# Optimization experiments

Hardware: AMD Instinct MI355X
Metric: run time of the kernel (lower is better)

Reference implementation:

```python
import jax, jax.numpy as jnp
import numpy as np

B = 16
Dv, Hv, Wv = 128, 128, 128   # patchsize voxel grid (C=1)
NPTS = 1920                  # 16*120 points
EPS_IN = 1e-5                # InstanceNorm eps


def _inorm(x):
    # InstanceNorm1d, affine=False: normalize over last (length) dim per (b, c)
    m = jnp.mean(x, axis=-1, keepdims=True)
    v = jnp.var(x, axis=-1, keepdims=True)
    return (x - m) * jax.lax.rsqrt(v + EPS_IN)


def _mlp(q, w1, b1, w2, b2, w3, b3, w4, b4, w5, b5):
    b = q.shape[0]
    x = q.reshape(b, 256, 8)                                    # (b, 2048//8, 8)
    x = jnp.einsum('bil,oi->bol', x, w1) + b1[None, :, None]    # Conv1d(256,240,1) -> (b,240,8)
    x = jax.nn.relu(_inorm(x.reshape(b, 64, 30)))               # view (b,64,30), IN(64)
    # Conv1d(64,128,1,groups=64): each in-ch -> 2 out-chs; then view (b,32,120)
    x = (x[:, :, None, :] * w2[None, :, :, None] + b2.reshape(1, 64, 2, 1)).reshape(b, 32, 120)
    x = jax.nn.relu(_inorm(x))
    # Conv1d(32,64,1,groups=32); view (b,16,480)
    x = (x[:, :, None, :] * w3[None, :, :, None] + b3.reshape(1, 32, 2, 1)).reshape(b, 16, 480)
    x = jax.nn.relu(_inorm(x))
    # Conv1d(16,64,1,groups=16); view (b,16,1920)
    x = (x[:, :, None, :] * w4[None, :, :, None] + b4.reshape(1, 16, 4, 1)).reshape(b, 16, 1920)
    x = jax.nn.relu(_inorm(x))
    return jnp.einsum('bil,oi->bol', x, w5) + b5[None, :, None]  # Conv1d(16,3,1) -> (b,3,1920)


def _splat(vals, grid):
    # True adjoint of 3D grid_sample (align_corners=False, zeros padding):
    # trilinear scatter-add of point values into the voxel grid.
    # vals: (b, N); grid: (b, N, 3) with (x, y, z) ~ (W, H, D) normalized coords.
    b, n = vals.shape
    px = ((grid[..., 0] + 1.0) * Wv - 1.0) * 0.5
    py = ((grid[..., 1] + 1.0) * Hv - 1.0) * 0.5
    pz = ((grid[..., 2] + 1.0) * Dv - 1.0) * 0.5
    x0f = jnp.floor(px); y0f = jnp.floor(py); z0f = jnp.floor(pz)
    fx = px - x0f; fy = py - y0f; fz = pz - z0f
    x0 = x0f.astype(jnp.int32); y0 = y0f.astype(jnp.int32); z0 = z0f.astype(jnp.int32)
    bidx = jnp.arange(b, dtype=jnp.int32)[:, None]
    out = jnp.zeros(b * Dv * Hv * Wv, dtype=vals.dtype)
    for dz in (0, 1):
        wz = fz if dz else (1.0 - fz)
        for dy in (0, 1):
            wy = fy if dy else (1.0 - fy)
            for dx in (0, 1):
                wx = fx if dx else (1.0 - fx)
                xi = x0 + dx; yi = y0 + dy; zi = z0 + dz
                w = wx * wy * wz * vals
                valid = (xi >= 0) & (xi < Wv) & (yi >= 0) & (yi < Hv) & (zi >= 0) & (zi < Dv)
                w = jnp.where(valid, w, 0.0)
                xi = jnp.clip(xi, 0, Wv - 1)
                yi = jnp.clip(yi, 0, Hv - 1)
                zi = jnp.clip(zi, 0, Dv - 1)
                flat = ((bidx * Dv + zi) * Hv + yi) * Wv + xi
                out = out.at[flat.ravel()].add(w.ravel())
    return out.reshape(b, 1, Dv, Hv, Wv)


def _avgpool3(x):
    # AvgPool3d(3, stride=1, padding=1, count_include_pad=True) as separable 1D averages
    for ax in (2, 3, 4):
        pad = [(1, 1) if i == ax else (0, 0) for i in range(5)]
        xp = jnp.pad(x, pad)
        n = x.shape[ax]
        x = (jax.lax.slice_in_dim(xp, 0, n, axis=ax)
             + jax.lax.slice_in_dim(xp, 1, n + 1, axis=ax)
             + jax.lax.slice_in_dim(xp, 2, n + 2, axis=ax)) / 3.0
    return x


def _smooth(x):
    return _avgpool3(_avgpool3(_avgpool3(x)))


def _forward(q, q_val, w1, b1, w2, b2, w3, b3, w4, b4, w5, b5):
    b = q.shape[0]
    q3 = _mlp(q, w1, b1, w2, b2, w3, b3, w4, b4, w5, b5)   # (b, 3, 1920)
    coords = jnp.tanh(q3)                                    # q0_coord
    grid = jnp.transpose(coords, (0, 2, 1))                  # (b, 1920, 3)
    vals = jnp.broadcast_to(jax.nn.sigmoid(q_val).reshape(1, NPTS), (b, NPTS))
    out = _splat(vals, grid)
    out0 = _splat(jnp.ones((b, NPTS), q.dtype), grid)
    return _smooth(out) / (_smooth(out0) + 0.001)


def setup_inputs() -> dict:
    key = jax.random.key(0)
    ks = jax.random.split(key, 12)
    sc = 0.1
    return {
        'q': jax.random.normal(ks[0], (B, 2048), jnp.float32),
        'q_val': jax.random.normal(ks[1], (1, 1, 16, 120), jnp.float32),
        'w1': jax.random.normal(ks[2], (240, 256), jnp.float32) * sc,
        'b1': jax.random.normal(ks[3], (240,), jnp.float32) * sc,
        'w2': jax.random.normal(ks[4], (64, 2), jnp.float32) * sc,
        'b2': jax.random.normal(ks[5], (128,), jnp.float32) * sc,
        'w3': jax.random.normal(ks[6], (32, 2), jnp.float32) * sc,
        'b3': jax.random.normal(ks[7], (64,), jnp.float32) * sc,
        'w4': jax.random.normal(ks[8], (16, 4), jnp.float32) * sc,
        'b4': jax.random.normal(ks[9], (64,), jnp.float32) * sc,
        'w5': jax.random.normal(ks[10], (3, 16), jnp.float32) * sc,
        'b5': jax.random.normal(ks[11], (3,), jnp.float32) * sc,
    }


def reference(q, q_val, w1, b1, w2, b2, w3, b3, w4, b4, w5, b5):
    return _forward(q, q_val, w1, b1, w2, b2, w3, b3, w4, b4, w5, b5)
```

## Files before the change

### kernel.cpp

```cpp
#include <hip/hip_runtime.h>
#include <cstddef>

#define NB 16
#define NVOX 128
#define NPT 1920
#define NPAIRS 32768

static __device__ __forceinline__ float2 f2(float a, float b) {
    float2 r; r.x = a; r.y = b; return r;
}

__global__ __launch_bounds__(256)
void zero_out(float4* __restrict__ out)
{
    int idx = blockIdx.x * 2048 + threadIdx.x;
    #pragma unroll
    for (int i = 0; i < 8; ++i)
        out[idx + i * 256] = make_float4(0.f, 0.f, 0.f, 0.f);
}

__global__ __launch_bounds__(256)
void mlp_stage1(const float* __restrict__ q, const float* __restrict__ w1,
                const float* __restrict__ b1, float* __restrict__ x1g)
{
    __shared__ float wrow[256];
    __shared__ float psum[256];
    const int o = blockIdx.x;
    const int t = threadIdx.x;

    wrow[t] = w1[o * 256 + t];
    __syncthreads();

    const int half = t >> 7;
    const int bl = t & 127;
    const int b = bl >> 3, l = bl & 7;
    const float* qb = q + b * 2048 + l + half * 1024;
    float s = 0.f;
    #pragma unroll 8
    for (int i = 0; i < 128; ++i)
        s = fmaf(wrow[half * 128 + i], qb[i * 8], s);
    psum[t] = s;
    __syncthreads();

    if (t < 128) {
        int bb = t >> 3, ll = t & 7;
        x1g[bb * 1920 + o * 8 + ll] = b1[o] + psum[t] + psum[t + 128];
    }
}

__global__ __launch_bounds__(256)
void mlp_tail(const float* __restrict__ x1g, const float* __restrict__ qval,
              const float* __restrict__ w2, const float* __restrict__ b2,
              const float* __restrict__ w3, const float* __restrict__ b3,
              const float* __restrict__ w4, const float* __restrict__ b4,
              const float* __restrict__ w5, const float* __restrict__ b5,
              float4* __restrict__ pts, unsigned char* __restrict__ flags)
{
    __shared__ float bufA[7680];
    __shared__ float bufC[3840];
    __shared__ float psum[256], psq[256];
    __shared__ float meanv[64], rstdv[64];
    __shared__ float m4[16], r4[16];

    const int b = blockIdx.x;
    const int t = threadIdx.x;

    for (int u = t; u < 1920; u += 256) bufA[u] = x1g[b * 1920 + u];
    __syncthreads();

    {
        int c = t >> 2, g = t & 3;
        float s = 0.f, s2 = 0.f;
        for (int p = g; p < 30; p += 4) { float v = bufA[c * 30 + p]; s += v; s2 += v * v; }
        psum[t] = s; psq[t] = s2;
    }
    __syncthreads();
    if (t < 64) {
        float s = 0.f, s2 = 0.f;
        for (int g = 0; g < 4; ++g) { s += psum[t * 4 + g]; s2 += psq[t * 4 + g]; }
        float m = s * (1.f / 30.f);
        float var = s2 * (1.f / 30.f) - m * m;
        meanv[t] = m; rstdv[t] = rsqrtf(var + 1e-5f);
    }
    __syncthreads();
    for (int k = t; k < 1920; k += 256) {
        int c = k / 30;
        bufA[k] = fmaxf((bufA[k] - meanv[c]) * rstdv[c], 0.f);
    }
    __syncthreads();

    for (int m = t; m < 3840; m += 256) {
        int c = m / 60;
        int r = m - c * 60;
        int j = r / 30;
        int p = r - j * 30;
        bufC[m] = fmaf(bufA[c * 30 + p], w2[c * 2 + j], b2[c * 2 + j]);
    }
    __syncthreads();
    {
        int c = t >> 3, g = t & 7;
        float s = 0.f, s2 = 0.f;
        for (int p = g; p < 120; p += 8) { float v = bufC[c * 120 + p]; s += v; s2 += v * v; }
        psum[t] = s; psq[t] = s2;
    }
    __syncthreads();
    if (t < 32) {
        float s = 0.f, s2 = 0.f;
        for (int g = 0; g < 8; ++g) { s += psum[t * 8 + g]; s2 += psq[t * 8 + g]; }
        float m = s * (1.f / 120.f);
        float var = s2 * (1.f / 120.f) - m * m;
        meanv[t] = m; rstdv[t] = rsqrtf(var + 1e-5f);
    }
    __syncthreads();
    for (int m = t; m < 3840; m += 256) {
        int c = m / 120;
        bufC[m] = fmaxf((bufC[m] - meanv[c]) * rstdv[c], 0.f);
    }
    __syncthreads();

    for (int m = t; m < 7680; m += 256) {
        int c = m / 240;
        int r = m - c * 240;
        int j = r / 120;
        int p = r - j * 120;
        bufA[m] = fmaf(bufC[c * 120 + p], w3[c * 2 + j], b3[c * 2 + j]);
    }
    __syncthreads();

    const int c3 = t >> 4, g3 = t & 15;
    {
        float s = 0.f, s2 = 0.f;
        for (int k = 0; k < 30; ++k) { float v = bufA[c3 * 480 + g3 + 16 * k]; s += v; s2 += v * v; }
        psum[t] = s; psq[t] = s2;
    }
    __syncthreads();
    if (t < 16) {
        float s = 0.f, s2 = 0.f;
        for (int g = 0; g < 16; ++g) { s += psum[t * 16 + g]; s2 += psq[t * 16 + g]; }
        float m = s * (1.f / 480.f);
        float var = s2 * (1.f / 480.f) - m * m;
        meanv[t] = m; rstdv[t] = rsqrtf(var + 1e-5f);
    }
    __syncthreads();
    {
        float m = meanv[c3], r = rstdv[c3];
        float s = 0.f, s2 = 0.f;
        for (int k = 0; k < 30; ++k) {
            int idx = c3 * 480 + g3 + 16 * k;
            float v = fmaxf((bufA[idx] - m) * r, 0.f);
            bufA[idx] = v; s += v; s2 += v * v;
        }
        psum[t] = s; psq[t] = s2;
    }
    __syncthreads();
    if (t < 16) {
        float s = 0.f, s2 = 0.f;
        for (int g = 0; g < 16; ++g) { s += psum[t * 16 + g]; s2 += psq[t * 16 + g]; }
        float sum4 = 0.f, sq4 = 0.f;
        for (int j = 0; j < 4; ++j) {
            float w = w4[t * 4 + j], bb = b4[t * 4 + j];
            sum4 += w * s + 480.f * bb;
            sq4  += w * w * s2 + 2.f * w * bb * s + 480.f * bb * bb;
        }
        float m = sum4 * (1.f / 1920.f);
        float var = sq4 * (1.f / 1920.f) - m * m;
        m4[t] = m; r4[t] = rsqrtf(var + 1e-5f);
    }
    __syncthreads();

    for (int l = t; l < NPT; l += 256) {
        int j = l / 480;
        int p = l - j * 480;
        float a0 = b5[0], a1 = b5[1], a2 = b5[2];
        #pragma unroll
        for (int c = 0; c < 16; ++c) {
            float xv = bufA[c * 480 + p];
            float x4 = fmaf(xv, w4[c * 4 + j], b4[c * 4 + j]);
            float h  = fmaxf((x4 - m4[c]) * r4[c], 0.f);
            a0 = fmaf(w5[c],      h, a0);
            a1 = fmaf(w5[16 + c], h, a1);
            a2 = fmaf(w5[32 + c], h, a2);
        }
        float px = tanhf(a0) * 64.f + 63.5f;
        float py = tanhf(a1) * 64.f + 63.5f;
        float pz = tanhf(a2) * 64.f + 63.5f;
        float val = 1.f / (1.f + expf(-qval[l]));

        float4 pv; pv.x = px; pv.y = py; pv.z = pz; pv.w = val;
        pts[b * NPT + l] = pv;

        int x0 = (int)floorf(px), y0 = (int)floorf(py), z0 = (int)floorf(pz);
        int xlo = max(0, x0 - 3), xhi = min(127, x0 + 4);
        int ylo = max(0, y0 - 3), yhi = min(127, y0 + 4);
        int zlo = max(0, z0 - 3), zhi = min(127, z0 + 4);
        if (xlo > xhi || ylo > yhi || zlo > zhi) continue;
        int txl = xlo >> 3, txh = xhi >> 3;
        int tyl = ylo >> 3, tyh = yhi >> 3;
        int tzl = zlo >> 3, tzh = zhi >> 3;
        for (int tz = tzl; tz <= tzh; ++tz)
            for (int ty = tyl; ty <= tyh; ++ty)
                for (int tx = txl; tx <= txh; ++tx)
                    flags[((b * 16 + tz) * 16 + ty) * 16 + tx] = 1;
    }
}

__global__ __launch_bounds__(256)
void compact_tiles(const unsigned char* __restrict__ flags,
                   int* __restrict__ count, int* __restrict__ list)
{
    int i = blockIdx.x * 256 + threadIdx.x;
    const unsigned short* fp = (const unsigned short*)flags;
    if (fp[i] != 0) {
        int pos = atomicAdd(count, 1);
        list[pos] = i;
    }
}

__device__ __forceinline__ void coef(int g, float& cm1, float& c0, float& cp1)
{
    cm1 = (g == 1 || g == 127) ? 5.f : 6.f;
    c0  = (g == 0 || g == 127) ? 4.f : 7.f;
    cp1 = (g == 0 || g == 126) ? 5.f : 6.f;
}

__global__ __launch_bounds__(512)
void tile_active(const float4* __restrict__ pts, const int* __restrict__ count,
                 const int* __restrict__ list, float* __restrict__ out)
{
    __shared__ float2 raw[14 * 14 * 22];
    __shared__ float2 zs[8 * 14 * 22];

    if ((int)blockIdx.x >= *count) return;
    const int code = list[blockIdx.x];
    const int pair = code & 7;
    const int ty   = (code >> 3) & 15;
    const int tz   = (code >> 7) & 15;
    const int b    = code >> 11;
    const int Tx = pair * 16, Ty = ty * 8, Tz = tz * 8;
    const int t = threadIdx.x;

    float* ob = out + (((size_t)(b * NVOX + Tz) * NVOX + Ty) * NVOX + Tx);

    for (int u = t; u < 14 * 14 * 22; u += 512) raw[u] = f2(0.f, 0.f);
    __syncthreads();

    const float4* pb = pts + b * NPT;
    for (int p = t; p < NPT; p += 512) {
        float4 pt = pb[p];
        float x0f = floorf(pt.x), y0f = floorf(pt.y), z0f = floorf(pt.z);
        int x0 = (int)x0f, y0 = (int)y0f, z0 = (int)z0f;
        int lx0 = x0 - Tx + 3, ly0 = y0 - Ty + 3, lz0 = z0 - Tz + 3;
        if (lx0 + 1 < 0 || lx0 > 21 || ly0 + 1 < 0 || ly0 > 13 ||
            lz0 + 1 < 0 || lz0 > 13) continue;
        float fx = pt.x - x0f, fy = pt.y - y0f, fz = pt.z - z0f;
        float val = pt.w;
        #pragma unroll
        for (int dz = 0; dz < 2; ++dz) {
            int zi = z0 + dz, lz = lz0 + dz;
            if ((unsigned)zi >= 128u || (unsigned)lz >= 14u) continue;
            float wz = dz ? fz : 1.f - fz;
            #pragma unroll
            for (int dy = 0; dy < 2; ++dy) {
                int yi = y0 + dy, ly = ly0 + dy;
                if ((unsigned)yi >= 128u || (unsigned)ly >= 14u) continue;
                float wy = dy ? fy : 1.f - fy;
                #pragma unroll
                for (int dx = 0; dx < 2; ++dx) {
                    int xi = x0 + dx, lx = lx0 + dx;
                    if ((unsigned)xi >= 128u || (unsigned)lx >= 22u) continue;
                    float w = (dx ? fx : 1.f - fx) * wy * wz;
                    float2* cell = &raw[(lz * 14 + ly) * 22 + lx];
                    atomicAdd(&cell->x, w * val);
                    atomicAdd(&cell->y, w);
                }
            }
        }
    }
    __syncthreads();

    for (int u = t; u < 8 * 14 * 22; u += 512) {
        int lx = u % 22;
        int tmp = u / 22;
        int ly = tmp % 14;
        int lz = tmp / 14;
        float cm1, c0, cp1; coef(Tz + lz, cm1, c0, cp1);
        const float2* a = &raw[(lz * 14 + ly) * 22 + lx];
        const int S = 14 * 22;
        float sx = (a[0].x + a[6 * S].x) + 3.f * (a[S].x + a[5 * S].x)
                 + cm1 * a[2 * S].x + c0 * a[3 * S].x + cp1 * a[4 * S].x;
        float sy = (a[0].y + a[6 * S].y) + 3.f * (a[S].y + a[5 * S].y)
                 + cm1 * a[2 * S].y + c0 * a[3 * S].y + cp1 * a[4 * S].y;
        zs[u] = f2(sx * (1.f / 27.f), sy * (1.f / 27.f));
    }
    __syncthreads();

    float2* ys = raw;
    for (int u = t; u < 8 * 8 * 22; u += 512) {
        int lx = u % 22;
        int tmp = u / 22;
        int ly = tmp % 8;
        int lz = tmp / 8;
        float cm1, c0, cp1; coef(Ty + ly, cm1, c0, cp1);
        const float2* a = &zs[(lz * 14 + ly) * 22 + lx];
        const int S = 22;
        float sx = (a[0].x + a[6 * S].x) + 3.f * (a[S].x + a[5 * S].x)
                 + cm1 * a[2 * S].x + c0 * a[3 * S].x + cp1 * a[4 * S].x;
        float sy = (a[0].y + a[6 * S].y) + 3.f * (a[S].y + a[5 * S].y)
                 + cm1 * a[2 * S].y + c0 * a[3 * S].y + cp1 * a[4 * S].y;
        ys[(lz * 8 + ly) * 22 + lx] = f2(sx * (1.f / 27.f), sy * (1.f / 27.f));
    }
    __syncthreads();

    for (int u = t; u < 16 * 8 * 8; u += 512) {
        int x = u & 15, y = (u >> 4) & 7, z = u >> 7;
        float cm1, c0, cp1; coef(Tx + x, cm1, c0, cp1);
        const float2* a = &ys[(z * 8 + y) * 22 + x];
        float sx = (a[0].x + a[6].x) + 3.f * (a[1].x + a[5].x)
                 + cm1 * a[2].x + c0 * a[3].x + cp1 * a[4].x;
        float sy = (a[0].y + a[6].y) + 3.f * (a[1].y + a[5].y)
                 + cm1 * a[2].y + c0 * a[3].y + cp1 * a[4].y;
        ob[((size_t)z * NVOX + y) * NVOX + x] =
            (sx * (1.f / 27.f)) / (sy * (1.f / 27.f) + 0.001f);
    }
}

extern "C" void kernel_launch(void* const* d_in, const int* in_sizes, int n_in,
                              void* d_out, int out_size, void* d_ws, size_t ws_size,
                              hipStream_t stream)
{
    const float* q    = (const float*)d_in[0];
    const float* qval = (const float*)d_in[1];
    const float* w1   = (const float*)d_in[2];
    const float* b1   = (const float*)d_in[3];
    const float* w2   = (const float*)d_in[4];
    const float* b2   = (const float*)d_in[5];
    const float* w3   = (const float*)d_in[6];
    const float* b3   = (const float*)d_in[7];
    const float* w4   = (const float*)d_in[8];
    const float* b4   = (const float*)d_in[9];
    const float* w5   = (const float*)d_in[10];
    const float* b5   = (const float*)d_in[11];
    float* out = (float*)d_out;

    unsigned char* flags = (unsigned char*)d_ws;
    int*    count = (int*)((char*)d_ws + 65536);
    int*    list  = (int*)((char*)d_ws + 65552);
    float4* pts   = (float4*)((char*)d_ws + 196624);
    float*  x1g   = (float*)((char*)d_ws + 688144);

    hipMemsetAsync(d_ws, 0, 65540, stream);

    zero_out<<<4096, 256, 0, stream>>>((float4*)out);

    mlp_stage1<<<240, 256, 0, stream>>>(q, w1, b1, x1g);

    mlp_tail<<<NB, 256, 0, stream>>>(x1g, qval, w2, b2, w3, b3,
                                     w4, b4, w5, b5, pts, flags);

    compact_tiles<<<NPAIRS / 256, 256, 0, stream>>>(flags, count, list);

    tile_active<<<NPAIRS, 512, 0, stream>>>(pts, count, list, out);
}
```

Before: 249.4 us.

## Fuse output zeroing and tile compaction into tile kernel; register-sliding smoothing passes

Removes the separate full-output zero kernel and the tile-compaction kernel. Each of the 32768 tile blocks now checks its own flag: inactive tiles write zeros directly and exit, while active tiles run the splat and smoothing. The three separable smoothing passes now run in place in one shared buffer, with each thread sliding a 7-tap register window and the final pass writing float4 stores. This avoids writing the output twice and cuts shared memory use, which may raise occupancy. The cost is a launch of all blocks, including the inactive ones, and some passes that use only a fraction of the threads.

```diff
diff --git a/kernel.cpp b/kernel.cpp
--- a/kernel.cpp
+++ b/kernel.cpp
@@ -8,15 +8,6 @@
 
 static __device__ __forceinline__ float2 f2(float a, float b) {
     float2 r; r.x = a; r.y = b; return r;
-}
-
-__global__ __launch_bounds__(256)
-void zero_out(float4* __restrict__ out)
-{
-    int idx = blockIdx.x * 2048 + threadIdx.x;
-    #pragma unroll
-    for (int i = 0; i < 8; ++i)
-        out[idx + i * 256] = make_float4(0.f, 0.f, 0.f, 0.f);
 }
 
 __global__ __launch_bounds__(256)
@@ -204,18 +195,6 @@
     }
 }
 
-__global__ __launch_bounds__(256)
-void compact_tiles(const unsigned char* __restrict__ flags,
-                   int* __restrict__ count, int* __restrict__ list)
-{
-    int i = blockIdx.x * 256 + threadIdx.x;
-    const unsigned short* fp = (const unsigned short*)flags;
-    if (fp[i] != 0) {
-        int pos = atomicAdd(count, 1);
-        list[pos] = i;
-    }
-}
-
 __device__ __forceinline__ void coef(int g, float& cm1, float& c0, float& cp1)
 {
     cm1 = (g == 1 || g == 127) ? 5.f : 6.f;
@@ -223,15 +202,14 @@
     cp1 = (g == 0 || g == 126) ? 5.f : 6.f;
 }
 
-__global__ __launch_bounds__(512)
-void tile_active(const float4* __restrict__ pts, const int* __restrict__ count,
-                 const int* __restrict__ list, float* __restrict__ out)
+__global__ __launch_bounds__(512, 8)
+void tile_all(const float4* __restrict__ pts,
+              const unsigned char* __restrict__ flags,
+              float* __restrict__ out)
 {
     __shared__ float2 raw[14 * 14 * 22];
-    __shared__ float2 zs[8 * 14 * 22];
-
-    if ((int)blockIdx.x >= *count) return;
-    const int code = list[blockIdx.x];
+
+    const int code = blockIdx.x;
     const int pair = code & 7;
     const int ty   = (code >> 3) & 15;
     const int tz   = (code >> 7) & 15;
@@ -241,7 +219,20 @@
 
     float* ob = out + (((size_t)(b * NVOX + Tz) * NVOX + Ty) * NVOX + Tx);
 
-    for (int u = t; u < 14 * 14 * 22; u += 512) raw[u] = f2(0.f, 0.f);
+    const unsigned short fl = ((const unsigned short*)flags)[code];
+    if (fl == 0) {
+        if (t < 256) {
+            int x4 = t & 3, y = (t >> 2) & 7, z = t >> 5;
+            *(float4*)&ob[((size_t)z * NVOX + y) * NVOX + x4 * 4] =
+                make_float4(0.f, 0.f, 0.f, 0.f);
+        }
+        return;
+    }
+
+    {
+        float4* rz = (float4*)raw;
+        for (int u = t; u < 2156; u += 512) rz[u] = make_float4(0.f, 0.f, 0.f, 0.f);
+    }
     __syncthreads();
 
     const float4* pb = pts + b * NPT;
@@ -278,49 +269,66 @@
     }
     __syncthreads();
 
-    for (int u = t; u < 8 * 14 * 22; u += 512) {
-        int lx = u % 22;
-        int tmp = u / 22;
-        int ly = tmp % 14;
-        int lz = tmp / 14;
-        float cm1, c0, cp1; coef(Tz + lz, cm1, c0, cp1);
-        const float2* a = &raw[(lz * 14 + ly) * 22 + lx];
-        const int S = 14 * 22;
-        float sx = (a[0].x + a[6 * S].x) + 3.f * (a[S].x + a[5 * S].x)
-                 + cm1 * a[2 * S].x + c0 * a[3 * S].x + cp1 * a[4 * S].x;
-        float sy = (a[0].y + a[6 * S].y) + 3.f * (a[S].y + a[5 * S].y)
-                 + cm1 * a[2 * S].y + c0 * a[3 * S].y + cp1 * a[4 * S].y;
-        zs[u] = f2(sx * (1.f / 27.f), sy * (1.f / 27.f));
-    }
-    __syncthreads();
-
-    float2* ys = raw;
-    for (int u = t; u < 8 * 8 * 22; u += 512) {
-        int lx = u % 22;
-        int tmp = u / 22;
-        int ly = tmp % 8;
-        int lz = tmp / 8;
-        float cm1, c0, cp1; coef(Ty + ly, cm1, c0, cp1);
-        const float2* a = &zs[(lz * 14 + ly) * 22 + lx];
-        const int S = 22;
-        float sx = (a[0].x + a[6 * S].x) + 3.f * (a[S].x + a[5 * S].x)
-                 + cm1 * a[2 * S].x + c0 * a[3 * S].x + cp1 * a[4 * S].x;
-        float sy = (a[0].y + a[6 * S].y) + 3.f * (a[S].y + a[5 * S].y)
-                 + cm1 * a[2 * S].y + c0 * a[3 * S].y + cp1 * a[4 * S].y;
-        ys[(lz * 8 + ly) * 22 + lx] = f2(sx * (1.f / 27.f), sy * (1.f / 27.f));
-    }
-    __syncthreads();
-
-    for (int u = t; u < 16 * 8 * 8; u += 512) {
-        int x = u & 15, y = (u >> 4) & 7, z = u >> 7;
-        float cm1, c0, cp1; coef(Tx + x, cm1, c0, cp1);
-        const float2* a = &ys[(z * 8 + y) * 22 + x];
-        float sx = (a[0].x + a[6].x) + 3.f * (a[1].x + a[5].x)
-                 + cm1 * a[2].x + c0 * a[3].x + cp1 * a[4].x;
-        float sy = (a[0].y + a[6].y) + 3.f * (a[1].y + a[5].y)
-                 + cm1 * a[2].y + c0 * a[3].y + cp1 * a[4].y;
-        ob[((size_t)z * NVOX + y) * NVOX + x] =
-            (sx * (1.f / 27.f)) / (sy * (1.f / 27.f) + 0.001f);
+    if (t < 308) {
+        float2 w0 = raw[t],           w1 = raw[t + 308],     w2 = raw[t + 2 * 308],
+               w3 = raw[t + 3 * 308], w4 = raw[t + 4 * 308], w5 = raw[t + 5 * 308],
+               w6 = raw[t + 6 * 308];
+        #pragma unroll
+        for (int z = 0; z < 8; ++z) {
+            float cm1, c0, cp1; coef(Tz + z, cm1, c0, cp1);
+            float sx = (w0.x + w6.x) + 3.f * (w1.x + w5.x)
+                     + cm1 * w2.x + c0 * w3.x + cp1 * w4.x;
+            float sy = (w0.y + w6.y) + 3.f * (w1.y + w5.y)
+                     + cm1 * w2.y + c0 * w3.y + cp1 * w4.y;
+            float2 nxt = raw[t + ((z < 7) ? z + 7 : 7) * 308];
+            raw[t + z * 308] = f2(sx * (1.f / 27.f), sy * (1.f / 27.f));
+            w0 = w1; w1 = w2; w2 = w3; w3 = w4; w4 = w5; w5 = w6; w6 = nxt;
+        }
+    }
+    __syncthreads();
+
+    if (t < 176) {
+        int z = t / 22, lx = t - z * 22;
+        float2* base = &raw[z * 308 + lx];
+        float2 w0 = base[0],      w1 = base[22],     w2 = base[2 * 22],
+               w3 = base[3 * 22], w4 = base[4 * 22], w5 = base[5 * 22],
+               w6 = base[6 * 22];
+        #pragma unroll
+        for (int y = 0; y < 8; ++y) {
+            float cm1, c0, cp1; coef(Ty + y, cm1, c0, cp1);
+            float sx = (w0.x + w6.x) + 3.f * (w1.x + w5.x)
+                     + cm1 * w2.x + c0 * w3.x + cp1 * w4.x;
+            float sy = (w0.y + w6.y) + 3.f * (w1.y + w5.y)
+                     + cm1 * w2.y + c0 * w3.y + cp1 * w4.y;
+            float2 nxt = base[((y < 7) ? y + 7 : 7) * 22];
+            base[y * 22] = f2(sx * (1.f / 27.f), sy * (1.f / 27.f));
+            w0 = w1; w1 = w2; w2 = w3; w3 = w4; w4 = w5; w5 = w6; w6 = nxt;
+        }
+    }
+    __syncthreads();
+
+    if (t < 128) {
+        int row = t >> 1, half = t & 1;
+        int z = row >> 3, y = row & 7;
+        const float2* a = &raw[z * 308 + y * 22 + half * 8];
+        float2 w0 = a[0], w1 = a[1], w2 = a[2], w3 = a[3],
+               w4 = a[4], w5 = a[5], w6 = a[6];
+        float res[8];
+        #pragma unroll
+        for (int i = 0; i < 8; ++i) {
+            int x = half * 8 + i;
+            float cm1, c0, cp1; coef(Tx + x, cm1, c0, cp1);
+            float sx = (w0.x + w6.x) + 3.f * (w1.x + w5.x)
+                     + cm1 * w2.x + c0 * w3.x + cp1 * w4.x;
+            float sy = (w0.y + w6.y) + 3.f * (w1.y + w5.y)
+                     + cm1 * w2.y + c0 * w3.y + cp1 * w4.y;
+            res[i] = (sx * (1.f / 27.f)) / (sy * (1.f / 27.f) + 0.001f);
+            float2 nxt = a[(i < 7) ? i + 7 : 13];
+            w0 = w1; w1 = w2; w2 = w3; w3 = w4; w4 = w5; w5 = w6; w6 = nxt;
+        }
+        float* orow = &ob[((size_t)z * NVOX + y) * NVOX + half * 8];
+        *(float4*)&orow[0] = make_float4(res[0], res[1], res[2], res[3]);
+        *(float4*)&orow[4] = make_float4(res[4], res[5], res[6], res[7]);
     }
 }
 
@@ -343,21 +351,15 @@
     float* out = (float*)d_out;
 
     unsigned char* flags = (unsigned char*)d_ws;
-    int*    count = (int*)((char*)d_ws + 65536);
-    int*    list  = (int*)((char*)d_ws + 65552);
-    float4* pts   = (float4*)((char*)d_ws + 196624);
-    float*  x1g   = (float*)((char*)d_ws + 688144);
-
-    hipMemsetAsync(d_ws, 0, 65540, stream);
-
-    zero_out<<<4096, 256, 0, stream>>>((float4*)out);
+    float4* pts = (float4*)((char*)d_ws + 65536);
+    float*  x1g = (float*)((char*)d_ws + 557056);
+
+    hipMemsetAsync(d_ws, 0, 65536, stream);
 
     mlp_stage1<<<240, 256, 0, stream>>>(q, w1, b1, x1g);
 
     mlp_tail<<<NB, 256, 0, stream>>>(x1g, qval, w2, b2, w3, b3,
                                      w4, b4, w5, b5, pts, flags);
 
-    compact_tiles<<<NPAIRS / 256, 256, 0, stream>>>(flags, count, list);
-
-    tile_active<<<NPAIRS, 512, 0, stream>>>(pts, count, list, out);
-}
+    tile_all<<<NPAIRS, 512, 0, stream>>>(pts, flags, out);
+}
```

Result: slower. 279.0 us (+11.9%).
